# Kernel tuning notes

Measured on AMD Instinct MI355X. Metric: run time of the kernel, lower is better.

The kernel has to match this reference:

```python
import jax, jax.numpy as jnp
import numpy as np

B, V = 256, 128000


def setup_inputs() -> dict:
    key = jax.random.key(0)
    k1, k2 = jax.random.split(key)
    logits = jax.random.normal(k1, (B, V), dtype=jnp.float32) * 4.0
    # temperatures in [0.3, 1.2] to avoid division by ~0
    temperatures = jax.random.uniform(k2, (B,), dtype=jnp.float32) * 0.9 + 0.3
    return {"logits": logits, "temperatures": temperatures}


def reference(logits, temperatures):
    # temperature-scaled softmax
    x = logits.astype(jnp.float32) / temperatures[:, None]
    probs = jax.nn.softmax(x, axis=-1)  # (B, V)
    # torch.empty_like(probs).exponential_(1).clamp_min_(1e-10)
    noise = jnp.maximum(
        jax.random.exponential(jax.random.key(42), probs.shape, dtype=jnp.float32),
        1e-10,
    )
    # Gumbel-max style sampling: argmax of probs / Exp(1) noise
    return jnp.argmax(probs / noise, axis=-1)  # (B,) int
```

## Files before the change

### kernel.cpp

```cpp
#include <hip/hip_runtime.h>
#include <stdint.h>
#include <math.h>

#define BB 256
#define ROW 128000
#define SPLIT 4
#define CHUNK (ROW / SPLIT)
#define THREADS 512
#define WAVES (THREADS / 64)
#define EPB (THREADS * 8)
#define FULL_ITERS 7
#define ITERS 8
#define GRID (BB * SPLIT)

#define TF_K2 0x1BD11BF0u
#define SMALL_BITS 0x00100000u
#define MIN_L 1.4426950408889634e-10f

__device__ __forceinline__ uint32_t rotl32(uint32_t x, int r) {
    return __builtin_amdgcn_alignbit(x, x, 32 - r);
}

__device__ __forceinline__ void threefry8_xor(uint32_t c, uint32_t bits[8]) {
    uint32_t x0[8], x1[8];
#pragma unroll
    for (int j = 0; j < 8; ++j) x1[j] = c + (uint32_t)(j + 42);

#pragma unroll
    for (int j = 0; j < 8; ++j) {
        x0[j] = x1[j];
        x1[j] = rotl32(x1[j], 13) ^ x0[j];
    }

#define RND(r)                                        \
    do {                                              \
        _Pragma("unroll")                             \
        for (int j = 0; j < 8; ++j) {                 \
            x0[j] += x1[j];                           \
            x1[j] = rotl32(x1[j], (r)) ^ x0[j];       \
        }                                             \
    } while (0)
#define RNDI(r, A, B)                                 \
    do {                                              \
        _Pragma("unroll")                             \
        for (int j = 0; j < 8; ++j) {                 \
            x1[j] += (B);                             \
            x0[j] = x0[j] + (A) + x1[j];              \
            x1[j] = rotl32(x1[j], (r)) ^ x0[j];       \
        }                                             \
    } while (0)

    RND(15); RND(26); RND(6);
    RNDI(17, 42u, TF_K2 + 1u);
    RND(29); RND(16); RND(24);
    RNDI(13, TF_K2, 2u);
    RND(15); RND(26); RND(6);
    RNDI(17, 0u, 45u);
    RND(29); RND(16); RND(24);
    RNDI(13, 42u, TF_K2 + 4u);
    RND(15); RND(26); RND(6);

#undef RND
#undef RNDI

#pragma unroll
    for (int j = 0; j < 8; ++j) bits[j] = (x0[j] + TF_K2) ^ (x1[j] + 5u);
}

__device__ __forceinline__ uint32_t f2o(float f) {
    uint32_t u = __float_as_uint(f);
    return (u & 0x80000000u) ? ~u : (u | 0x80000000u);
}

__device__ __forceinline__ void do_slab(const float xs[8], uint32_t cb, int t,
                                        float invT2, float& best_s,
                                        int& best_code) {
    uint32_t bits[8];
    threefry8_xor(cb, bits);

    float L8[8];
#pragma unroll
    for (int j = 0; j < 8; ++j) {
        const float uf = __uint_as_float(0x3F800000u | (bits[j] >> 9));
        L8[j] = __builtin_amdgcn_logf(2.0f - uf);
    }

    const uint32_t b01 = min(min(bits[0], bits[1]), bits[2]);
    const uint32_t b34 = min(min(bits[3], bits[4]), bits[5]);
    const uint32_t b67 = min(bits[6], bits[7]);
    const uint32_t bmin = min(min(b01, b34), b67);
    if (__any(bmin < SMALL_BITS)) {
#pragma unroll
        for (int j = 0; j < 8; ++j) {
            const float uf = __uint_as_float(0x3F800000u | (bits[j] >> 9));
            const float u = uf - 1.0f;
            const float es2 = u * fmaf(u, fmaf(u, fmaf(u,
                -0.3606737602222408f, -0.4808983469629878f),
                -0.7213475204444817f), -1.4426950408889634f);
            const float es2c = fminf(es2, -MIN_L);
            L8[j] = (bits[j] < SMALL_BITS) ? es2c : L8[j];
        }
    }

#pragma unroll
    for (int j = 0; j < 8; ++j) {
        const float lg = __builtin_amdgcn_logf(-L8[j]);
        const float s = fmaf(xs[j], invT2, -lg);
        if (s > best_s) { best_s = s; best_code = t * 8 + j; }
    }
}

__global__ __launch_bounds__(THREADS, 4) void sampler_kernel(
    const float* __restrict__ logits,
    const float* __restrict__ temps,
    unsigned long long* __restrict__ ws) {
    const int g = blockIdx.x;
    const int b = g >> 2;
    const int q = g & 3;
    const float invT2 = 1.0f / (temps[b] * 0.69314718055994530942f);
    const float* rowp = logits + (size_t)b * ROW + (size_t)q * CHUNK;
    const uint32_t cbase = (uint32_t)b * (uint32_t)ROW + (uint32_t)q * CHUNK;

    float best_s = -INFINITY;
    int best_code = 0;
    const int tid = threadIdx.x;

#pragma unroll 1
    for (int t = 0; t < FULL_ITERS; ++t) {
        const int vl = t * EPB + tid * 8;
        const float4 xa = *reinterpret_cast<const float4*>(rowp + vl);
        const float4 xb = *reinterpret_cast<const float4*>(rowp + vl + 4);
        const float xs[8] = {xa.x, xa.y, xa.z, xa.w, xb.x, xb.y, xb.z, xb.w};
        do_slab(xs, cbase + (uint32_t)vl, t, invT2, best_s, best_code);
    }
    {
        const int vl = FULL_ITERS * EPB + tid * 8;
        if (vl < CHUNK) {
            const float4 xa = *reinterpret_cast<const float4*>(rowp + vl);
            const float4 xb = *reinterpret_cast<const float4*>(rowp + vl + 4);
            const float xs[8] = {xa.x, xa.y, xa.z, xa.w,
                                 xb.x, xb.y, xb.z, xb.w};
            do_slab(xs, cbase + (uint32_t)vl, FULL_ITERS, invT2, best_s,
                    best_code);
        }
    }

    const uint32_t best_v = (uint32_t)(q * CHUNK + tid * 8) +
                            (uint32_t)((best_code >> 3) * EPB) +
                            (uint32_t)(best_code & 7);

    unsigned long long best =
        ((unsigned long long)f2o(best_s) << 32) | (uint32_t)(~best_v);

#pragma unroll
    for (int off = 32; off >= 1; off >>= 1) {
        const unsigned long long o = __shfl_xor(best, off);
        best = (o > best) ? o : best;
    }

    __shared__ unsigned long long sbest[WAVES];
    const int lane = tid & 63;
    const int wid = tid >> 6;
    if (lane == 0) sbest[wid] = best;
    __syncthreads();

    if (tid == 0) {
        unsigned long long r = sbest[0];
#pragma unroll
        for (int w = 1; w < WAVES; ++w) r = (sbest[w] > r) ? sbest[w] : r;
        ws[g] = r;
    }
}

__global__ __launch_bounds__(BB) void combine_kernel(
    const unsigned long long* __restrict__ ws, int* __restrict__ out) {
    const int b = threadIdx.x;
    const unsigned long long* p = ws + b * SPLIT;
    unsigned long long r = p[0];
#pragma unroll
    for (int w = 1; w < SPLIT; ++w) r = (p[w] > r) ? p[w] : r;
    out[b] = (int)(~(uint32_t)(r & 0xFFFFFFFFull));
}

extern "C" void kernel_launch(void* const* d_in, const int* in_sizes, int n_in,
                              void* d_out, int out_size, void* d_ws, size_t ws_size,
                              hipStream_t stream) {
    const float* logits = (const float*)d_in[0];
    const float* temps = (const float*)d_in[1];
    int* out = (int*)d_out;
    unsigned long long* ws = (unsigned long long*)d_ws;

    hipLaunchKernelGGL(sampler_kernel, dim3(GRID), dim3(THREADS), 0, stream,
                       logits, temps, ws);
    hipLaunchKernelGGL(combine_kernel, dim3(1), dim3(BB), 0, stream, ws, out);
}
```

Baseline: 87.48 us.

## Prune Gumbel-max candidates with a sampled lower bound before generating noise

Adds a seed kernel that scores a strided sample of each row to get a lower bound on the row's maximum score. The main kernel splits each row 16 ways and keeps only logits that could still beat that bound, given the clamp-limited maximum noise contribution. It queues the survivors in shared memory and runs Threefry plus the log math only on them, falling back to full evaluation if the queue overflows. The goal is to avoid RNG and transcendental work on most elements. The cost is an extra launch, ballot and atomic compaction overhead, and a weaker filter at high temperatures, where many rows may take the fallback path.

New measurement: 88.48 us. Within noise of the previous version (+1.1%).

```diff
diff --git a/kernel.cpp b/kernel.cpp
--- a/kernel.cpp
+++ b/kernel.cpp
@@ -4,51 +4,66 @@
 
 #define BB 256
 #define ROW 128000
-#define SPLIT 4
+#define SPLIT 16
 #define CHUNK (ROW / SPLIT)
 #define THREADS 512
 #define WAVES (THREADS / 64)
 #define EPB (THREADS * 8)
-#define FULL_ITERS 7
-#define ITERS 8
 #define GRID (BB * SPLIT)
+#define CAP 6144
+
+#define SEED_THREADS 256
+#define SEED_STRIDE 496
 
 #define TF_K2 0x1BD11BF0u
 #define SMALL_BITS 0x00100000u
 #define MIN_L 1.4426950408889634e-10f
+#define LN2 0.69314718055994530942f
+#define GMAX 33.0f
 
 __device__ __forceinline__ uint32_t rotl32(uint32_t x, int r) {
     return __builtin_amdgcn_alignbit(x, x, 32 - r);
 }
 
+#define R1S(r)        { x0 += x1; x1 = rotl32(x1, (r)) ^ x0; }
+#define RI1S(r, A, B) { x1 += (B); x0 = x0 + (A) + x1; x1 = rotl32(x1, (r)) ^ x0; }
+
+__device__ __forceinline__ uint32_t threefry1_xor(uint32_t c) {
+    uint32_t x1 = c + 42u;
+    uint32_t x0 = x1;
+    x1 = rotl32(x1, 13) ^ x0;
+    R1S(15) R1S(26) R1S(6)
+    RI1S(17, 42u, TF_K2 + 1u)
+    R1S(29) R1S(16) R1S(24)
+    RI1S(13, TF_K2, 2u)
+    R1S(15) R1S(26) R1S(6)
+    RI1S(17, 0u, 45u)
+    R1S(29) R1S(16) R1S(24)
+    RI1S(13, 42u, TF_K2 + 4u)
+    R1S(15) R1S(26) R1S(6)
+    return (x0 + TF_K2) ^ (x1 + 5u);
+}
+
 __device__ __forceinline__ void threefry8_xor(uint32_t c, uint32_t bits[8]) {
     uint32_t x0[8], x1[8];
 #pragma unroll
     for (int j = 0; j < 8; ++j) x1[j] = c + (uint32_t)(j + 42);
-
-#pragma unroll
-    for (int j = 0; j < 8; ++j) {
-        x0[j] = x1[j];
-        x1[j] = rotl32(x1[j], 13) ^ x0[j];
-    }
+#pragma unroll
+    for (int j = 0; j < 8; ++j) { x0[j] = x1[j]; x1[j] = rotl32(x1[j], 13) ^ x0[j]; }
 
 #define RND(r)                                        \
-    do {                                              \
-        _Pragma("unroll")                             \
+    do { _Pragma("unroll")                            \
         for (int j = 0; j < 8; ++j) {                 \
             x0[j] += x1[j];                           \
             x1[j] = rotl32(x1[j], (r)) ^ x0[j];       \
-        }                                             \
-    } while (0)
+        } } while (0)
 #define RNDI(r, A, B)                                 \
-    do {                                              \
-        _Pragma("unroll")                             \
+    do { _Pragma("unroll")                            \
         for (int j = 0; j < 8; ++j) {                 \
             x1[j] += (B);                             \
             x0[j] = x0[j] + (A) + x1[j];              \
             x1[j] = rotl32(x1[j], (r)) ^ x0[j];       \
-        }                                             \
-    } while (0)
+        } } while (0)
 
     RND(15); RND(26); RND(6);
     RNDI(17, 42u, TF_K2 + 1u);
@@ -59,12 +74,27 @@
     RND(29); RND(16); RND(24);
     RNDI(13, 42u, TF_K2 + 4u);
     RND(15); RND(26); RND(6);
-
 #undef RND
 #undef RNDI
 
 #pragma unroll
     for (int j = 0; j < 8; ++j) bits[j] = (x0[j] + TF_K2) ^ (x1[j] + 5u);
+}
+
+__device__ __forceinline__ float noise_negL(uint32_t bits) {
+    const float uf = __uint_as_float(0x3F800000u | (bits >> 9));
+    const float L = __builtin_amdgcn_logf(2.0f - uf);
+    const float u = uf - 1.0f;
+    const float es2 = u * fmaf(u, fmaf(u, fmaf(u,
+        -0.3606737602222408f, -0.4808983469629878f),
+        -0.7213475204444817f), -1.4426950408889634f);
+    const float es2c = fminf(es2, -MIN_L);
+    return (bits < SMALL_BITS) ? es2c : L;
+}
+
+__device__ __forceinline__ float score1(float x, float invT2, uint32_t bits) {
+    const float L = noise_negL(bits);
+    return fmaf(x, invT2, -__builtin_amdgcn_logf(-L));
 }
 
 __device__ __forceinline__ uint32_t f2o(float f) {
@@ -72,110 +102,174 @@
     return (u & 0x80000000u) ? ~u : (u | 0x80000000u);
 }
 
-__device__ __forceinline__ void do_slab(const float xs[8], uint32_t cb, int t,
-                                        float invT2, float& best_s,
-                                        int& best_code) {
+__global__ __launch_bounds__(SEED_THREADS) void seed_kernel(
+    const float* __restrict__ logits,
+    const float* __restrict__ temps,
+    float* __restrict__ gs) {
+    const int b = blockIdx.x;
+    const int t = threadIdx.x;
+    const float invT2 = 1.0f / (temps[b] * LN2);
+    const int off = t * SEED_STRIDE;
+    const float* rowp = logits + (size_t)b * ROW + off;
+    const uint32_t cb = (uint32_t)b * ROW + (uint32_t)off;
+
+    const float4 xa = *reinterpret_cast<const float4*>(rowp);
+    const float4 xb = *reinterpret_cast<const float4*>(rowp + 4);
+    const float xs[8] = {xa.x, xa.y, xa.z, xa.w, xb.x, xb.y, xb.z, xb.w};
     uint32_t bits[8];
     threefry8_xor(cb, bits);
 
-    float L8[8];
-#pragma unroll
-    for (int j = 0; j < 8; ++j) {
-        const float uf = __uint_as_float(0x3F800000u | (bits[j] >> 9));
-        L8[j] = __builtin_amdgcn_logf(2.0f - uf);
-    }
-
-    const uint32_t b01 = min(min(bits[0], bits[1]), bits[2]);
-    const uint32_t b34 = min(min(bits[3], bits[4]), bits[5]);
-    const uint32_t b67 = min(bits[6], bits[7]);
-    const uint32_t bmin = min(min(b01, b34), b67);
-    if (__any(bmin < SMALL_BITS)) {
-#pragma unroll
-        for (int j = 0; j < 8; ++j) {
-            const float uf = __uint_as_float(0x3F800000u | (bits[j] >> 9));
-            const float u = uf - 1.0f;
-            const float es2 = u * fmaf(u, fmaf(u, fmaf(u,
-                -0.3606737602222408f, -0.4808983469629878f),
-                -0.7213475204444817f), -1.4426950408889634f);
-            const float es2c = fminf(es2, -MIN_L);
-            L8[j] = (bits[j] < SMALL_BITS) ? es2c : L8[j];
-        }
-    }
-
-#pragma unroll
-    for (int j = 0; j < 8; ++j) {
-        const float lg = __builtin_amdgcn_logf(-L8[j]);
-        const float s = fmaf(xs[j], invT2, -lg);
-        if (s > best_s) { best_s = s; best_code = t * 8 + j; }
-    }
+    float bs = -INFINITY;
+#pragma unroll
+    for (int j = 0; j < 8; ++j) bs = fmaxf(bs, score1(xs[j], invT2, bits[j]));
+
+#pragma unroll
+    for (int off2 = 32; off2 >= 1; off2 >>= 1)
+        bs = fmaxf(bs, __shfl_xor(bs, off2));
+
+    __shared__ float sred[SEED_THREADS / 64];
+    const int lane = t & 63, wid = t >> 6;
+    if (lane == 0) sred[wid] = bs;
+    __syncthreads();
+    if (t == 0)
+        gs[b] = fmaxf(fmaxf(sred[0], sred[1]), fmaxf(sred[2], sred[3]));
 }
 
 __global__ __launch_bounds__(THREADS, 4) void sampler_kernel(
     const float* __restrict__ logits,
     const float* __restrict__ temps,
-    unsigned long long* __restrict__ ws) {
+    const float* __restrict__ gs,
+    unsigned long long* __restrict__ parts) {
+    __shared__ int scnt;
+    __shared__ unsigned short qidx[CAP];
+    __shared__ float qx[CAP];
+    __shared__ unsigned long long sbest[WAVES];
+
     const int g = blockIdx.x;
-    const int b = g >> 2;
-    const int q = g & 3;
-    const float invT2 = 1.0f / (temps[b] * 0.69314718055994530942f);
+    const int b = g >> 4;
+    const int q = g & 15;
+    const float T = temps[b];
+    const float invT2 = 1.0f / (T * LN2);
+    const float xthr = (gs[b] - GMAX) * (T * LN2);
     const float* rowp = logits + (size_t)b * ROW + (size_t)q * CHUNK;
-    const uint32_t cbase = (uint32_t)b * (uint32_t)ROW + (uint32_t)q * CHUNK;
-
+    const uint32_t cbase = (uint32_t)b * ROW + (uint32_t)(q * CHUNK);
+    const int tid = threadIdx.x;
+    const int lane = tid & 63;
+    const unsigned long long lmask_lt = (1ull << lane) - 1ull;
+
+    if (tid == 0) scnt = 0;
+    __syncthreads();
+
+    float xs0[8], xs1[8];
+    {
+        const int rel = tid * 8;
+        const float4 xa = *reinterpret_cast<const float4*>(rowp + rel);
+        const float4 xb = *reinterpret_cast<const float4*>(rowp + rel + 4);
+        xs0[0]=xa.x; xs0[1]=xa.y; xs0[2]=xa.z; xs0[3]=xa.w;
+        xs0[4]=xb.x; xs0[5]=xb.y; xs0[6]=xb.z; xs0[7]=xb.w;
+#pragma unroll
+        for (int j = 0; j < 8; ++j) {
+            const bool pass = xs0[j] > xthr;
+            const unsigned long long mk = __ballot(pass);
+            if (mk != 0ull) {
+                int base = 0;
+                if (lane == 0) base = atomicAdd(&scnt, __popcll(mk));
+                base = __builtin_amdgcn_readfirstlane(base);
+                if (pass) {
+                    const int pos = base + (int)__popcll(mk & lmask_lt);
+                    if (pos < CAP) {
+                        qidx[pos] = (unsigned short)(rel + j);
+                        qx[pos] = xs0[j];
+                    }
+                }
+            }
+        }
+    }
+    const int rel1 = EPB + tid * 8;
+    const bool in1 = rel1 < CHUNK;
+    if (in1) {
+        const float4 xa = *reinterpret_cast<const float4*>(rowp + rel1);
+        const float4 xb = *reinterpret_cast<const float4*>(rowp + rel1 + 4);
+        xs1[0]=xa.x; xs1[1]=xa.y; xs1[2]=xa.z; xs1[3]=xa.w;
+        xs1[4]=xb.x; xs1[5]=xb.y; xs1[6]=xb.z; xs1[7]=xb.w;
+#pragma unroll
+        for (int j = 0; j < 8; ++j) {
+            const bool pass = xs1[j] > xthr;
+            const unsigned long long mk = __ballot(pass);
+            if (mk != 0ull) {
+                int base = 0;
+                if (lane == 0) base = atomicAdd(&scnt, __popcll(mk));
+                base = __builtin_amdgcn_readfirstlane(base);
+                if (pass) {
+                    const int pos = base + (int)__popcll(mk & lmask_lt);
+                    if (pos < CAP) {
+                        qidx[pos] = (unsigned short)(rel1 + j);
+                        qx[pos] = xs1[j];
+                    }
+                }
+            }
+        }
+    }
+    __syncthreads();
+
+    const int total = scnt;
     float best_s = -INFINITY;
-    int best_code = 0;
-    const int tid = threadIdx.x;
-
-#pragma unroll 1
-    for (int t = 0; t < FULL_ITERS; ++t) {
-        const int vl = t * EPB + tid * 8;
-        const float4 xa = *reinterpret_cast<const float4*>(rowp + vl);
-        const float4 xb = *reinterpret_cast<const float4*>(rowp + vl + 4);
-        const float xs[8] = {xa.x, xa.y, xa.z, xa.w, xb.x, xb.y, xb.z, xb.w};
-        do_slab(xs, cbase + (uint32_t)vl, t, invT2, best_s, best_code);
-    }
-    {
-        const int vl = FULL_ITERS * EPB + tid * 8;
-        if (vl < CHUNK) {
-            const float4 xa = *reinterpret_cast<const float4*>(rowp + vl);
-            const float4 xb = *reinterpret_cast<const float4*>(rowp + vl + 4);
-            const float xs[8] = {xa.x, xa.y, xa.z, xa.w,
-                                 xb.x, xb.y, xb.z, xb.w};
-            do_slab(xs, cbase + (uint32_t)vl, FULL_ITERS, invT2, best_s,
-                    best_code);
-        }
-    }
-
-    const uint32_t best_v = (uint32_t)(q * CHUNK + tid * 8) +
-                            (uint32_t)((best_code >> 3) * EPB) +
-                            (uint32_t)(best_code & 7);
+    uint32_t best_rel = 0u;
+
+    if (total > CAP) {
+        {
+            const int rel = tid * 8;
+            uint32_t bits[8];
+            threefry8_xor(cbase + (uint32_t)rel, bits);
+#pragma unroll
+            for (int j = 0; j < 8; ++j) {
+                const float s = score1(xs0[j], invT2, bits[j]);
+                if (s > best_s) { best_s = s; best_rel = (uint32_t)(rel + j); }
+            }
+        }
+        if (in1) {
+            uint32_t bits[8];
+            threefry8_xor(cbase + (uint32_t)rel1, bits);
+#pragma unroll
+            for (int j = 0; j < 8; ++j) {
+                const float s = score1(xs1[j], invT2, bits[j]);
+                if (s > best_s) { best_s = s; best_rel = (uint32_t)(rel1 + j); }
+            }
+        }
+    } else {
+        for (int i = tid; i < total; i += THREADS) {
+            const int rel = (int)qidx[i];
+            const float x = qx[i];
+            const uint32_t bits = threefry1_xor(cbase + (uint32_t)rel);
+            const float s = score1(x, invT2, bits);
+            if (s > best_s) { best_s = s; best_rel = (uint32_t)rel; }
+        }
+    }
+
+    const uint32_t best_v = (uint32_t)(q * CHUNK) + best_rel;
 
     unsigned long long best =
         ((unsigned long long)f2o(best_s) << 32) | (uint32_t)(~best_v);
-
 #pragma unroll
     for (int off = 32; off >= 1; off >>= 1) {
         const unsigned long long o = __shfl_xor(best, off);
         best = (o > best) ? o : best;
     }
-
-    __shared__ unsigned long long sbest[WAVES];
-    const int lane = tid & 63;
     const int wid = tid >> 6;
     if (lane == 0) sbest[wid] = best;
     __syncthreads();
-
     if (tid == 0) {
         unsigned long long r = sbest[0];
 #pragma unroll
         for (int w = 1; w < WAVES; ++w) r = (sbest[w] > r) ? sbest[w] : r;
-        ws[g] = r;
+        parts[g] = r;
     }
 }
 
 __global__ __launch_bounds__(BB) void combine_kernel(
-    const unsigned long long* __restrict__ ws, int* __restrict__ out) {
+    const unsigned long long* __restrict__ parts, int* __restrict__ out) {
     const int b = threadIdx.x;
-    const unsigned long long* p = ws + b * SPLIT;
+    const unsigned long long* p = parts + b * SPLIT;
     unsigned long long r = p[0];
 #pragma unroll
     for (int w = 1; w < SPLIT; ++w) r = (p[w] > r) ? p[w] : r;
@@ -188,9 +282,12 @@
     const float* logits = (const float*)d_in[0];
     const float* temps = (const float*)d_in[1];
     int* out = (int*)d_out;
-    unsigned long long* ws = (unsigned long long*)d_ws;
-
+    float* gs = (float*)d_ws;
+    unsigned long long* parts = (unsigned long long*)((char*)d_ws + 1024);
+
+    hipLaunchKernelGGL(seed_kernel, dim3(BB), dim3(SEED_THREADS), 0, stream,
+                       logits, temps, gs);
     hipLaunchKernelGGL(sampler_kernel, dim3(GRID), dim3(THREADS), 0, stream,
-                       logits, temps, ws);
-    hipLaunchKernelGGL(combine_kernel, dim3(1), dim3(BB), 0, stream, ws, out);
-}
+                       logits, temps, gs, parts);
+    hipLaunchKernelGGL(combine_kernel, dim3(1), dim3(BB), 0, stream, parts, out);
+}
```
